# Kernel optimization log

Measured on AMD Instinct MI355X. Metric: run time of the kernel, lower is better.

The kernel has to match this reference:

```python
import jax, jax.numpy as jnp
import numpy as np

N = 8192        # total nodes in the batch of graphs
E = 262144      # edges (avg degree 32)
F_IN = 128      # input node features
G = 64          # graphs in batch
C = 10          # classes
K1, K2, K3 = 4096, 2048, 1024  # int(0.5*N), int(0.5*K1), int(0.5*K2)


def setup_inputs() -> dict:
    key = jax.random.key(0)
    ks = jax.random.split(key, 16)
    def lin(k, i, o):
        return jax.random.normal(k, (i, o), jnp.float32) / np.float32(np.sqrt(i))
    return {
        "x": jax.random.normal(ks[0], (N, F_IN), jnp.float32),
        "edge_index": jax.random.randint(ks[1], (2, E), 0, N),
        "batch": jnp.sort(jax.random.randint(ks[2], (N,), 0, G)),
        "W1": lin(ks[3], F_IN, 32), "b1": jnp.zeros((32,), jnp.float32),
        "W2": lin(ks[4], 32, 64),   "b2": jnp.zeros((64,), jnp.float32),
        "W3": lin(ks[5], 64, 128),  "b3": jnp.zeros((128,), jnp.float32),
        "W4": lin(ks[6], 128, 256), "b4": jnp.zeros((256,), jnp.float32),
        "W5": lin(ks[7], 384, 128), "b5": jnp.zeros((128,), jnp.float32),
        "W6": lin(ks[8], 192, 64),  "b6": jnp.zeros((64,), jnp.float32),
        "W7": lin(ks[9], 96, 32),   "b7": jnp.zeros((32,), jnp.float32),
        "p1": jax.random.normal(ks[10], (32,), jnp.float32),
        "p2": jax.random.normal(ks[11], (64,), jnp.float32),
        "p3": jax.random.normal(ks[12], (128,), jnp.float32),
        "Wl1": lin(ks[13], 64, 64),
        "Wc": lin(ks[14], 64, C), "bc": jnp.zeros((C,), jnp.float32),
    }


def _gcn(A, x, W, b):
    # PyG GCNConv (improved=False): out = D^-1/2 (A+I) D^-1/2 propagated src->dst.
    n = A.shape[0]
    Ah = A + jnp.eye(n, dtype=A.dtype)
    deg = Ah.sum(axis=0)                                  # degree at targets (cols)
    dinv = jnp.where(deg > 0, deg ** -0.5, 0.0).astype(A.dtype)
    An = dinv[:, None] * Ah * dinv[None, :]               # edge norm d[src]^-.5 * d[dst]^-.5
    return An.T @ (x @ W) + b                             # out[dst] += norm * (xW)[src]


def _gpool(A, x, p, k):
    # GPool: scores = Linear(x)/||p||, top-k select, gate by sigmoid, reindex dense adj.
    scores = (x @ p) / jnp.linalg.norm(p)                 # [n]
    vals, idx = jax.lax.top_k(scores, k)
    xp = x[idx] * jax.nn.sigmoid(vals)[:, None]
    Ap = (A[idx][:, idx] > 0).astype(x.dtype)             # dense_to_sparse rebinarizes
    return xp, Ap, idx


def reference(x, edge_index, batch, W1, b1, W2, b2, W3, b3, W4, b4, W5, b5,
              W6, b6, W7, b7, p1, p2, p3, Wl1, Wc, bc):
    elu = jax.nn.elu
    # to_dense_adj: dense N x N adjacency (duplicate edges accumulate)
    A = jnp.zeros((N, N), x.dtype).at[edge_index[0], edge_index[1]].add(1.0)
    x1 = elu(_gcn(A, x, W1, b1))
    x2, A2, i2 = _gpool(A, x1, p1, K1); x2 = elu(x2)
    x3 = elu(_gcn(A2, x2, W2, b2))
    x4, A4, i4 = _gpool(A2, x3, p2, K2); x4 = elu(x4)
    x5 = elu(_gcn(A4, x4, W3, b3))
    x6, A6, i6 = _gpool(A4, x5, p3, K3); x6 = elu(x6)
    x7 = elu(_gcn(A6, x6, W4, b4))
    u = jnp.zeros((K2, x7.shape[1]), x7.dtype).at[i6].set(x7)   # GUnpool
    x8 = elu(jnp.concatenate([u, x5], axis=1))
    x9 = elu(_gcn(A4, x8, W5, b5))
    u = jnp.zeros((K1, x9.shape[1]), x9.dtype).at[i4].set(x9)
    x10 = elu(jnp.concatenate([u, x3], axis=1))
    x11 = elu(_gcn(A2, x10, W6, b6))
    u = jnp.zeros((N, x11.shape[1]), x11.dtype).at[i2].set(x11)
    x12 = elu(jnp.concatenate([u, x1], axis=1))
    x13 = elu(_gcn(A, x12, W7, b7))
    gmax = jax.ops.segment_max(x13, batch, num_segments=G)      # global max pool
    gsum = jax.ops.segment_sum(x13, batch, num_segments=G)
    cnt = jax.ops.segment_sum(jnp.ones((N, 1), x13.dtype), batch, num_segments=G)
    h = elu(jnp.concatenate([gmax, gsum / cnt], axis=1))        # [G, 64]
    h = elu(h @ Wl1)
    return jax.nn.log_softmax(h @ Wc + bc, axis=-1)
```

## Files before the change

kernel.cpp:

```cpp
#include <hip/hip_runtime.h>
#include <math.h>

#define NN 8192
#define EE 262144
#define GG 64
#define CC 10
#define KK1 4096
#define KK2 2048
#define KK3 1024
#define PITCH 128

typedef unsigned long long ull;

__device__ __forceinline__ float eluf(float x) { return x > 0.f ? x : expm1f(x); }
__device__ __forceinline__ float sigf(float x) { return 1.f / (1.f + expf(-x)); }
__device__ __forceinline__ unsigned f2s(float f) {
    unsigned u = __float_as_uint(f);
    return (u & 0x80000000u) ? ~u : (u | 0x80000000u);
}

__global__ void k_init(const int* __restrict__ ei, int* __restrict__ cnt1,
                       int* __restrict__ csr1, const int* __restrict__ batch,
                       int* __restrict__ gstart, const float* __restrict__ X,
                       const float* __restrict__ W, float* __restrict__ Y) {
    __shared__ float Xs[32][33];
    __shared__ float Ws[32][36];
    int tid = threadIdx.x;
    if ((int)blockIdx.x >= 1024) {
        int txn = tid & 7, tym = tid >> 3;
        int m0 = ((int)blockIdx.x - 1024) * 32;
        float4 acc = make_float4(0.f, 0.f, 0.f, 0.f);
        for (int k0 = 0; k0 < 128; k0 += 32) {
            int r = tid >> 3, c4 = (tid & 7) << 2;
            *(float4*)&Xs[r][c4] = *(const float4*)&X[(size_t)(m0 + r) * 128 + k0 + c4];
            *(float4*)&Ws[r][c4] = *(const float4*)&W[(size_t)(k0 + r) * 32 + c4];
            __syncthreads();
#pragma unroll 8
            for (int kk = 0; kk < 32; kk++) {
                float4 wv = *(const float4*)&Ws[kk][txn * 4];
                float xv = Xs[tym][kk];
                acc.x += xv * wv.x; acc.y += xv * wv.y;
                acc.z += xv * wv.z; acc.w += xv * wv.w;
            }
            __syncthreads();
        }
        *(float4*)&Y[(size_t)(m0 + tym) * 32 + txn * 4] = acc;
        return;
    }
    int e = blockIdx.x * 256 + tid;
    int s = ei[e], d = ei[EE + e];
    int pos = atomicAdd(&cnt1[d], 1);
    csr1[(d << 7) + pos] = s;
    if (e < NN) {
        int g = batch[e];
        int prev = (e == 0) ? -1 : batch[e - 1];
        for (int gg = prev + 1; gg <= g; gg++) gstart[gg] = e;
        if (e == NN - 1)
            for (int gg = g + 1; gg <= GG; gg++) gstart[gg] = NN;
    }
}

template<int KPOOL, int F, int FOUT, int L1>
__global__ void k_pool_gemm_sub(const float* __restrict__ x, const float* __restrict__ score,
                                const int* __restrict__ idx, float* __restrict__ xW,
                                const float* __restrict__ W,
                                const int* __restrict__ csrP, const int* __restrict__ roffP,
                                const int* __restrict__ degP,
                                const int* __restrict__ invmap,
                                int* __restrict__ csrO, int* __restrict__ roffO,
                                int* __restrict__ degO, float* __restrict__ dinvO) {
    constexpr int MT = KPOOL / 32, NT = FOUT / 32, NPOOL = MT * NT;
    int tid = threadIdx.x;
    if ((int)blockIdx.x < NPOOL) {
        __shared__ float Xs[32][F + 4];
        __shared__ float Ws[32][36];
        __shared__ float sfac[32];
        __shared__ int sIdx[32];
        int mt = (int)blockIdx.x % MT, nt = (int)blockIdx.x / MT;
        int m0 = mt * 32, n0 = nt * 32;
        if (tid < 32) {
            int j = idx[m0 + tid];
            sIdx[tid] = j;
            sfac[tid] = sigf(score[j]);
        }
        __syncthreads();
        for (int i4 = tid; i4 < 32 * (F / 4); i4 += 256) {
            int r = i4 / (F / 4), c = i4 % (F / 4);
            float4 v = *(const float4*)&x[(size_t)sIdx[r] * F + c * 4];
            float sf = sfac[r];
            v.x = eluf(v.x * sf); v.y = eluf(v.y * sf);
            v.z = eluf(v.z * sf); v.w = eluf(v.w * sf);
            *(float4*)&Xs[r][c * 4] = v;
        }
        __syncthreads();
        int txn = tid & 7, tym = tid >> 3;
        float4 acc = make_float4(0.f, 0.f, 0.f, 0.f);
        for (int k0 = 0; k0 < F; k0 += 32) {
            {
                int r = tid >> 3, c4 = (tid & 7) << 2;
                *(float4*)&Ws[r][c4] = *(const float4*)&W[(size_t)(k0 + r) * FOUT + n0 + c4];
            }
            __syncthreads();
#pragma unroll 8
            for (int kk = 0; kk < 32; kk++) {
                float4 wv = *(const float4*)&Ws[kk][txn * 4];
                float xv = Xs[tym][k0 + kk];
                acc.x += xv * wv.x; acc.y += xv * wv.y;
                acc.z += xv * wv.z; acc.w += xv * wv.w;
            }
            __syncthreads();
        }
        *(float4*)&xW[(size_t)(m0 + tym) * FOUT + n0 + txn * 4] = acc;
        return;
    }
    int wid = (((int)blockIdx.x - NPOOL) * 256 + tid) >> 6;
    int lane = tid & 63;
    if (wid >= KPOOL) return;
    int j = idx[wid];
    int cnt = 0;
    if (L1) {
        int j0 = j << 7;
        int len = degP[j];
        int e0 = (lane < len) ? csrP[j0 + lane] : -1;
        int e1 = (64 + lane < len) ? csrP[j0 + 64 + lane] : -1;
        bool dup0 = false, dup1 = false;
        for (int q = 0; q < len - 1; q++) {
            int vq = (q < 64) ? __shfl(e0, q, 64) : __shfl(e1, q - 64, 64);
            if (lane > q && e0 == vq) dup0 = true;
            if (64 + lane > q && e1 == vq) dup1 = true;
        }
        {
            bool sel = (lane < len) && !dup0;
            int val = 0;
            if (sel) { int v = invmap[e0]; if (v > 0) val = v - 1; else sel = false; }
            ull m = __ballot(sel);
            if (sel) { int off = __popcll(m & ((1ull << lane) - 1ull)); csrO[j0 + cnt + off] = val; }
            cnt += __popcll(m);
        }
        {
            bool sel = (64 + lane < len) && !dup1;
            int val = 0;
            if (sel) { int v = invmap[e1]; if (v > 0) val = v - 1; else sel = false; }
            ull m = __ballot(sel);
            if (sel) { int off = __popcll(m & ((1ull << lane) - 1ull)); csrO[j0 + cnt + off] = val; }
            cnt += __popcll(m);
        }
        if (lane == 0) {
            roffO[wid] = j0;
            degO[wid] = cnt;
            dinvO[wid] = 1.f / sqrtf((float)(cnt + 1));
        }
    } else {
        int j0 = roffP[j];
        int len = degP[j];
        for (int base = 0; base < len; base += 64) {
            bool sel = false;
            int val = 0;
            if (base + lane < len) {
                int e = csrP[j0 + base + lane];
                int v = invmap[e];
                if (v > 0) { sel = true; val = v - 1; }
            }
            ull m = __ballot(sel);
            if (sel) { int off = __popcll(m & ((1ull << lane) - 1ull)); csrO[j0 + cnt + off] = val; }
            cnt += __popcll(m);
        }
        if (lane == 0) {
            roffO[wid] = j0;
            degO[wid] = cnt;
            dinvO[wid] = 1.f / sqrtf((float)(cnt + 1));
        }
    }
}

__global__ void k_gemm_up(const float* __restrict__ xl, const int* __restrict__ inv,
                          const float* __restrict__ xr, int Fl, int Fr,
                          const float* __restrict__ W, float* __restrict__ Y,
                          int M, int K, int F) {
    __shared__ float Xs[32][33];
    __shared__ float Ws[32][36];
    __shared__ int sIdx[32];
    int tid = threadIdx.x;
    int txn = tid & 7, tym = tid >> 3;
    int m0 = blockIdx.x * 32, n0 = blockIdx.y * 32;
    if (tid < 32) sIdx[tid] = inv[m0 + tid];
    float4 acc = make_float4(0.f, 0.f, 0.f, 0.f);
    __syncthreads();
    for (int k0 = 0; k0 < K; k0 += 32) {
        {
            int r = tid >> 3, c4 = (tid & 7) << 2;
            int kk = k0 + c4;
            float4 v;
            if (kk < Fl) {
                int rr = sIdx[r];
                v = (rr > 0) ? *(const float4*)&xl[(size_t)(rr - 1) * Fl + kk]
                             : make_float4(0.f, 0.f, 0.f, 0.f);
            } else {
                v = *(const float4*)&xr[(size_t)(m0 + r) * Fr + (kk - Fl)];
            }
            v.x = eluf(v.x); v.y = eluf(v.y); v.z = eluf(v.z); v.w = eluf(v.w);
            *(float4*)&Xs[r][c4] = v;
            *(float4*)&Ws[r][c4] = *(const float4*)&W[(size_t)(k0 + r) * F + n0 + c4];
        }
        __syncthreads();
#pragma unroll 8
        for (int kk = 0; kk < 32; kk++) {
            float4 wv = *(const float4*)&Ws[kk][txn * 4];
            float xv = Xs[tym][kk];
            acc.x += xv * wv.x; acc.y += xv * wv.y;
            acc.z += xv * wv.z; acc.w += xv * wv.w;
        }
        __syncthreads();
    }
    *(float4*)&Y[(size_t)(m0 + tym) * F + n0 + txn * 4] = acc;
}

template<int LOGF, int SCORE, int L1, int LS>
__global__ void k_prop(const int* __restrict__ csr, const int* __restrict__ roff,
                       const int* __restrict__ deg, const float* __restrict__ dinv,
                       const float* __restrict__ xW, const float* __restrict__ b,
                       float* __restrict__ xout, const float* __restrict__ p,
                       float* __restrict__ score) {
    constexpr int FQ = 1 << (LOGF - 2);
    constexpr int S = 1 << LS;
    constexpr int RL = FQ * S;
    const float4* xW4 = (const float4*)xW;
    int t = blockIdx.x * 256 + threadIdx.x;
    int d = t >> (LOGF - 2 + LS);
    int rem = t & (RL - 1);
    int q = rem >> LS, h = rem & (S - 1);
    int j0 = L1 ? (d << 7) : roff[d];
    int dg = deg[d];
    int j1 = j0 + dg;
    float dd = L1 ? (1.f / sqrtf((float)(dg + 1))) : dinv[d];
    int idx = (d << (LOGF - 2)) + q;
    float4 sum;
    if (h == 0) {
        float4 v0 = xW4[idx];
        sum = make_float4(dd * v0.x, dd * v0.y, dd * v0.z, dd * v0.w);
    } else {
        sum = make_float4(0.f, 0.f, 0.f, 0.f);
    }
    for (int j = j0 + h; j < j1; j += S) {
        int s = csr[j];
        float ds = L1 ? (1.f / sqrtf((float)(deg[s] + 1))) : dinv[s];
        float4 xv = xW4[(s << (LOGF - 2)) + q];
        sum.x += ds * xv.x; sum.y += ds * xv.y;
        sum.z += ds * xv.z; sum.w += ds * xv.w;
    }
#pragma unroll
    for (int m = 1; m < S; m <<= 1) {
        sum.x += __shfl_xor(sum.x, m, 64);
        sum.y += __shfl_xor(sum.y, m, 64);
        sum.z += __shfl_xor(sum.z, m, 64);
        sum.w += __shfl_xor(sum.w, m, 64);
    }
    float4 bv = *(const float4*)&b[q << 2];
    float4 o;
    o.x = eluf(dd * sum.x + bv.x);
    o.y = eluf(dd * sum.y + bv.y);
    o.z = eluf(dd * sum.z + bv.z);
    o.w = eluf(dd * sum.w + bv.w);
    if (h == 0) ((float4*)xout)[idx] = o;
    if (SCORE) {
        float4 pv = *(const float4*)&p[q << 2];
        float sc = 0.f, nr = 0.f;
        if (h == 0) {
            sc = o.x * pv.x + o.y * pv.y + o.z * pv.z + o.w * pv.w;
            nr = pv.x * pv.x + pv.y * pv.y + pv.z * pv.z + pv.w * pv.w;
        }
#pragma unroll
        for (int m = RL >> 1; m >= 1; m >>= 1) {
            sc += __shfl_xor(sc, m, 64);
            nr += __shfl_xor(nr, m, 64);
        }
        if (rem == 0) score[d] = sc / sqrtf(nr);
    }
}

__device__ __forceinline__ ull cex_shfl(ull v, int st, bool takeMax) {
    ull pv = __shfl_xor(v, st, 64);
    return takeMax ? (v > pv ? v : pv) : (v < pv ? v : pv);
}
__device__ __forceinline__ void cexr(ull& a, ull& b, bool desc) {
    if (desc ? (a < b) : (a > b)) { ull x = a; a = b; b = x; }
}

__global__ void k_topk_f(const float* __restrict__ score, ull* __restrict__ keys,
                         int N, int k, int* __restrict__ out_idx,
                         int* __restrict__ invmap, int* __restrict__ ctr) {
    __shared__ ull sk[4096];
    int tid = threadIdx.x;
    int bid = blockIdx.x;
    int nb = N >> 11;
    {
        int base = bid << 11;
        int giA = base + tid, giB = giA + 1024;
        ull a = ((ull)f2s(score[giA]) << 32) | (unsigned)(~giA);
        ull b = ((ull)f2s(score[giB]) << 32) | (unsigned)(~giB);
        for (int sz = 2; sz <= 2048; sz <<= 1) {
            int st = sz >> 1;
            if (st >= 64) {
                sk[tid] = a; sk[tid + 1024] = b;
                __syncthreads();
                for (; st >= 64; st >>= 1) {
                    int i = ((tid & ~(st - 1)) << 1) | (tid & (st - 1));
                    int j = i | st;
                    ull u = sk[i], v = sk[j];
                    bool desc = (((base + i) & sz) == 0);
                    if (desc ? (u < v) : (u > v)) { sk[i] = v; sk[j] = u; }
                    __syncthreads();
                }
                a = sk[tid]; b = sk[tid + 1024];
            }
            for (; st >= 1; st >>= 1) {
                bool low = (tid & st) == 0;
                a = cex_shfl(a, st, ((giA & sz) == 0) == low);
                b = cex_shfl(b, st, ((giB & sz) == 0) == low);
            }
        }
        if (nb == 1) {
            if (giA < k) { int j = (int)(~(unsigned)(a & 0xFFFFFFFFu)); out_idx[giA] = j; invmap[j] = giA + 1; }
            if (giB < k) { int j = (int)(~(unsigned)(b & 0xFFFFFFFFu)); out_idx[giB] = j; invmap[j] = giB + 1; }
            return;
        }
        keys[giA] = a; keys[giB] = b;
    }
    __syncthreads();
    if (tid == 0) { __threadfence(); atomicAdd(ctr, 1); }

    if (N == 4096) {
        if (bid != 0) return;
        if (tid == 0) { while (atomicAdd(ctr, 0) < 2) ; __threadfence(); }
        __syncthreads();
        ull a0 = keys[tid],        a1 = keys[tid + 1024];
        ull a2 = keys[tid + 2048], a3 = keys[tid + 3072];
        cexr(a0, a2, true); cexr(a1, a3, true);
        sk[tid] = a0; sk[tid + 1024] = a1;
        __syncthreads();
        for (int st = 1024; st >= 64; st >>= 1) {
            int i = ((tid & ~(st - 1)) << 1) | (tid & (st - 1));
            int j = i | st;
            ull u = sk[i], v = sk[j];
            if (u < v) { sk[i] = v; sk[j] = u; }
            __syncthreads();
        }
        a0 = sk[tid]; a1 = sk[tid + 1024];
        for (int st = 32; st >= 1; st >>= 1) {
            bool low = (tid & st) == 0;
            a0 = cex_shfl(a0, st, low);
            a1 = cex_shfl(a1, st, low);
        }
        int p, j;
        p = tid;        j = (int)(~(unsigned)(a0 & 0xFFFFFFFFu)); out_idx[p] = j; invmap[j] = p + 1;
        p = tid + 1024; j = (int)(~(unsigned)(a1 & 0xFFFFFFFFu)); out_idx[p] = j; invmap[j] = p + 1;
        return;
    }

    if (bid >= 2) return;
    if (tid == 0) { while (atomicAdd(ctr, 0) < 4) ; __threadfence(); }
    __syncthreads();
    {
        int base = bid << 12;
        bool desc = ((base & 4096) == 0);
        ull k0 = keys[base + tid], k1 = keys[base + tid + 1024];
        ull k2 = keys[base + tid + 2048], k3 = keys[base + tid + 3072];
        cexr(k0, k2, desc); cexr(k1, k3, desc);
        sk[tid] = k0; sk[tid + 1024] = k1; sk[tid + 2048] = k2; sk[tid + 3072] = k3;
        __syncthreads();
        for (int st = 1024; st >= 64; st >>= 1) {
            for (int pp = tid; pp < 2048; pp += 1024) {
                int i = ((pp & ~(st - 1)) << 1) | (pp & (st - 1));
                int j = i | st;
                ull u = sk[i], v = sk[j];
                if (desc ? (u < v) : (u > v)) { sk[i] = v; sk[j] = u; }
            }
            __syncthreads();
        }
        k0 = sk[tid]; k1 = sk[tid + 1024]; k2 = sk[tid + 2048]; k3 = sk[tid + 3072];
        for (int st = 32; st >= 1; st >>= 1) {
            bool low = (tid & st) == 0;
            k0 = cex_shfl(k0, st, desc == low);
            k1 = cex_shfl(k1, st, desc == low);
            k2 = cex_shfl(k2, st, desc == low);
            k3 = cex_shfl(k3, st, desc == low);
        }
        keys[base + tid] = k0; keys[base + tid + 1024] = k1;
        keys[base + tid + 2048] = k2; keys[base + tid + 3072] = k3;
    }
    __syncthreads();
    if (tid == 0) { __threadfence(); atomicAdd(ctr, 1); }
    if (bid != 0) return;
    if (tid == 0) { while (atomicAdd(ctr, 0) < 6) ; __threadfence(); }
    __syncthreads();
    {
        ull a0 = keys[tid],        a1 = keys[tid + 1024];
        ull a2 = keys[tid + 2048], a3 = keys[tid + 3072];
        ull b0 = keys[tid + 4096], b1 = keys[tid + 5120];
        ull b2 = keys[tid + 6144], b3 = keys[tid + 7168];
        cexr(a0, b0, true); cexr(a1, b1, true);
        cexr(a2, b2, true); cexr(a3, b3, true);
        cexr(a0, a2, true); cexr(a1, a3, true);
        sk[tid] = a0; sk[tid + 1024] = a1; sk[tid + 2048] = a2; sk[tid + 3072] = a3;
        __syncthreads();
        for (int st = 1024; st >= 64; st >>= 1) {
            for (int pp = tid; pp < 2048; pp += 1024) {
                int i = ((pp & ~(st - 1)) << 1) | (pp & (st - 1));
                int j = i | st;
                ull u = sk[i], v = sk[j];
                if (u < v) { sk[i] = v; sk[j] = u; }
            }
            __syncthreads();
        }
        a0 = sk[tid]; a1 = sk[tid + 1024]; a2 = sk[tid + 2048]; a3 = sk[tid + 3072];
        for (int st = 32; st >= 1; st >>= 1) {
            bool low = (tid & st) == 0;
            a0 = cex_shfl(a0, st, low);
            a1 = cex_shfl(a1, st, low);
            a2 = cex_shfl(a2, st, low);
            a3 = cex_shfl(a3, st, low);
        }
        int p, j;
        p = tid;        j = (int)(~(unsigned)(a0 & 0xFFFFFFFFu)); out_idx[p] = j; invmap[j] = p + 1;
        p = tid + 1024; j = (int)(~(unsigned)(a1 & 0xFFFFFFFFu)); out_idx[p] = j; invmap[j] = p + 1;
        p = tid + 2048; j = (int)(~(unsigned)(a2 & 0xFFFFFFFFu)); out_idx[p] = j; invmap[j] = p + 1;
        p = tid + 3072; j = (int)(~(unsigned)(a3 & 0xFFFFFFFFu)); out_idx[p] = j; invmap[j] = p + 1;
    }
}

__global__ void k_finale(const float* __restrict__ x13, const int* __restrict__ gstart,
                         const float* __restrict__ Wl1, const float* __restrict__ Wc,
                         const float* __restrict__ bc, float* __restrict__ out) {
    __shared__ float sm[8][32], ss[8][32];
    __shared__ float h0[64], h1[64], lg[CC];
    int g = blockIdx.x;
    int j0 = gstart[g], j1 = gstart[g + 1];
    int t = threadIdx.x;
    int f = t & 31, r = t >> 5;
    float m = -INFINITY, s = 0.f;
    for (int j = j0 + r; j < j1; j += 8) {
        float v = x13[(j << 5) + f];
        m = fmaxf(m, v);
        s += v;
    }
    sm[r][f] = m; ss[r][f] = s;
    __syncthreads();
    if (t < 32) {
        float mm = sm[0][t], sss = ss[0][t];
        for (int i = 1; i < 8; i++) { mm = fmaxf(mm, sm[i][t]); sss += ss[i][t]; }
        h0[t] = eluf(mm);
        h0[32 + t] = eluf(sss / (float)(j1 - j0));
    }
    __syncthreads();
    if (t < 64) {
        float sum = 0.f;
        for (int kk = 0; kk < 64; kk++) sum += h0[kk] * Wl1[kk * 64 + t];
        h1[t] = eluf(sum);
    }
    __syncthreads();
    if (t < CC) {
        float sum = bc[t];
        for (int kk = 0; kk < 64; kk++) sum += h1[kk] * Wc[kk * CC + t];
        lg[t] = sum;
    }
    __syncthreads();
    if (t == 0) {
        float mm = -1e30f;
        for (int c = 0; c < CC; c++) mm = fmaxf(mm, lg[c]);
        float se = 0.f;
        for (int c = 0; c < CC; c++) se += expf(lg[c] - mm);
        float lse = mm + logf(se);
        for (int c = 0; c < CC; c++) out[g * CC + c] = lg[c] - lse;
    }
}

extern "C" void kernel_launch(void* const* d_in, const int* in_sizes, int n_in,
                              void* d_out, int out_size, void* d_ws, size_t ws_size,
                              hipStream_t stream) {
    const float* x = (const float*)d_in[0];
    const int* ei = (const int*)d_in[1];
    const int* batch = (const int*)d_in[2];
    const float* W1 = (const float*)d_in[3];  const float* b1 = (const float*)d_in[4];
    const float* W2 = (const float*)d_in[5];  const float* b2 = (const float*)d_in[6];
    const float* W3 = (const float*)d_in[7];  const float* b3 = (const float*)d_in[8];
    const float* W4 = (const float*)d_in[9];  const float* b4 = (const float*)d_in[10];
    const float* W5 = (const float*)d_in[11]; const float* b5 = (const float*)d_in[12];
    const float* W6 = (const float*)d_in[13]; const float* b6 = (const float*)d_in[14];
    const float* W7 = (const float*)d_in[15]; const float* b7 = (const float*)d_in[16];
    const float* p1 = (const float*)d_in[17];
    const float* p2 = (const float*)d_in[18];
    const float* p3 = (const float*)d_in[19];
    const float* Wl1 = (const float*)d_in[20];
    const float* Wc = (const float*)d_in[21];
    const float* bc = (const float*)d_in[22];
    float* out = (float*)d_out;
    (void)in_sizes; (void)n_in; (void)out_size; (void)ws_size;

    char* w = (char*)d_ws;
    size_t off = 0;
    auto alloc = [&](size_t bytes) -> char* {
        char* p = w + off;
        off = (off + bytes + 255) & ~(size_t)255;
        return p;
    };

    size_t zero_begin = off;
    int* cnt1 = (int*)alloc(NN * 4);
    int* pos2 = (int*)alloc(NN * 4);
    int* inv4 = (int*)alloc(KK1 * 4);
    int* inv6 = (int*)alloc(KK2 * 4);
    int* tkctr = (int*)alloc(2 * 4);
    size_t zero_len = off - zero_begin;

    float* dinv2 = (float*)alloc(KK1 * 4);
    float* dinv3 = (float*)alloc(KK2 * 4);
    float* dinv4 = (float*)alloc(KK3 * 4);
    int* roff2 = (int*)alloc(KK1 * 4); int* deg2 = (int*)alloc(KK1 * 4);
    int* roff3 = (int*)alloc(KK2 * 4); int* deg3 = (int*)alloc(KK2 * 4);
    int* roff4 = (int*)alloc(KK3 * 4); int* deg4 = (int*)alloc(KK3 * 4);
    int* csr1 = (int*)alloc((size_t)NN * PITCH * 4);
    int* csr2 = (int*)alloc((size_t)NN * PITCH * 4);
    int* csr3 = (int*)alloc((size_t)NN * PITCH * 4);
    int* csr4 = (int*)alloc((size_t)NN * PITCH * 4);
    float* xW = (float*)alloc((size_t)262144 * 4);
    float* x1 = (float*)alloc((size_t)NN * 32 * 4);
    float* x3 = (float*)alloc((size_t)KK1 * 64 * 4);
    float* x5 = (float*)alloc((size_t)KK2 * 128 * 4);
    float* x7 = (float*)alloc((size_t)KK3 * 256 * 4);
    float* x9 = (float*)alloc((size_t)KK2 * 128 * 4);
    float* x11 = (float*)alloc((size_t)KK1 * 64 * 4);
    float* x13 = (float*)alloc((size_t)NN * 32 * 4);
    float* score1 = (float*)alloc(NN * 4);
    float* score2 = (float*)alloc(KK1 * 4);
    float* score3 = (float*)alloc(KK2 * 4);
    int* i2 = (int*)alloc(KK1 * 4);
    int* i4 = (int*)alloc(KK2 * 4);
    int* i6 = (int*)alloc(KK3 * 4);
    ull* keys = (ull*)alloc((size_t)NN * 8);
    int* gstart = (int*)alloc((GG + 1) * 4);

    hipMemsetAsync(w + zero_begin, 0, zero_len, stream);

    const int B = 256;
    k_init<<<1280, B, 0, stream>>>(ei, cnt1, csr1, batch, gstart, x, W1, xW);

    k_prop<5, 1, 1, 3><<<2048, B, 0, stream>>>(csr1, nullptr, cnt1, nullptr, xW, b1,
                                               x1, p1, score1);

    k_topk_f<<<4, 1024, 0, stream>>>(score1, keys, NN, KK1, i2, pos2, tkctr);
    k_pool_gemm_sub<KK1, 32, 64, 1><<<256 + KK1 / 4, B, 0, stream>>>(
        x1, score1, i2, xW, W2, csr1, nullptr, cnt1, pos2, csr2, roff2, deg2, dinv2);

    k_prop<6, 1, 0, 2><<<1024, B, 0, stream>>>(csr2, roff2, deg2, dinv2, xW, b2,
                                               x3, p2, score2);

    k_topk_f<<<2, 1024, 0, stream>>>(score2, keys, KK1, KK2, i4, inv4, tkctr + 1);
    k_pool_gemm_sub<KK2, 64, 128, 0><<<256 + KK2 / 4, B, 0, stream>>>(
        x3, score2, i4, xW, W3, csr2, roff2, deg2, inv4, csr3, roff3, deg3, dinv3);

    k_prop<7, 1, 0, 1><<<512, B, 0, stream>>>(csr3, roff3, deg3, dinv3, xW, b3,
                                              x5, p3, score3);

    k_topk_f<<<1, 1024, 0, stream>>>(score3, keys, KK2, KK3, i6, inv6, nullptr);
    k_pool_gemm_sub<KK3, 128, 256, 0><<<256 + KK3 / 4, B, 0, stream>>>(
        x5, score3, i6, xW, W4, csr3, roff3, deg3, inv6, csr4, roff4, deg4, dinv4);

    k_prop<8, 0, 0, 1><<<512, B, 0, stream>>>(csr4, roff4, deg4, dinv4, xW, b4,
                                              x7, nullptr, nullptr);

    k_gemm_up<<<dim3(KK2 / 32, 4), B, 0, stream>>>(x7, inv6, x5, 256, 128,
                                                   W5, xW, KK2, 384, 128);
    k_prop<7, 0, 0, 2><<<1024, B, 0, stream>>>(csr3, roff3, deg3, dinv3, xW, b5,
                                               x9, nullptr, nullptr);

    k_gemm_up<<<dim3(KK1 / 32, 2), B, 0, stream>>>(x9, inv4, x3, 128, 64,
                                                   W6, xW, KK1, 192, 64);
    k_prop<6, 0, 0, 2><<<1024, B, 0, stream>>>(csr2, roff2, deg2, dinv2, xW, b6,
                                               x11, nullptr, nullptr);

    k_gemm_up<<<dim3(NN / 32, 1), B, 0, stream>>>(x11, pos2, x1, 64, 32,
                                                  W7, xW, NN, 96, 32);
    k_prop<5, 0, 1, 3><<<2048, B, 0, stream>>>(csr1, nullptr, cnt1, nullptr, xW, b7,
                                               x13, nullptr, nullptr);

    k_finale<<<GG, B, 0, stream>>>(x13, gstart, Wl1, Wc, bc, out);
}
```

Before: 310.3 us.

## Fuse final GCN propagation with per-graph pooling and classifier head

Result: slower. 366.3 us (+18.0%).

```diff
diff --git a/kernel.cpp b/kernel.cpp
--- a/kernel.cpp
+++ b/kernel.cpp
@@ -275,6 +275,119 @@
             nr += __shfl_xor(nr, m, 64);
         }
         if (rem == 0) score[d] = sc / sqrtf(nr);
+    }
+}
+
+__global__ void k_prop7(const int* __restrict__ csr, const int* __restrict__ deg,
+                        const float* __restrict__ xW, const float* __restrict__ b,
+                        float* __restrict__ x13, const int* __restrict__ batch,
+                        const int* __restrict__ gstart, int* __restrict__ garr,
+                        const float* __restrict__ Wl1, const float* __restrict__ Wc,
+                        const float* __restrict__ bc, float* __restrict__ out) {
+    const float4* xW4 = (const float4*)xW;
+    int tid = threadIdx.x;
+    int t = blockIdx.x * 256 + tid;
+    int d = t >> 6;
+    int rem = t & 63;
+    int q = rem >> 3, h = rem & 7;
+    int j0 = d << 7;
+    int dg = deg[d];
+    int j1 = j0 + dg;
+    float dd = 1.f / sqrtf((float)(dg + 1));
+    int idx = (d << 3) + q;
+    float4 sum;
+    if (h == 0) {
+        float4 v0 = xW4[idx];
+        sum = make_float4(dd * v0.x, dd * v0.y, dd * v0.z, dd * v0.w);
+    } else {
+        sum = make_float4(0.f, 0.f, 0.f, 0.f);
+    }
+    for (int j = j0 + h; j < j1; j += 8) {
+        int s = csr[j];
+        float ds = 1.f / sqrtf((float)(deg[s] + 1));
+        float4 xv = xW4[(s << 3) + q];
+        sum.x += ds * xv.x; sum.y += ds * xv.y;
+        sum.z += ds * xv.z; sum.w += ds * xv.w;
+    }
+#pragma unroll
+    for (int m = 1; m < 8; m <<= 1) {
+        sum.x += __shfl_xor(sum.x, m, 64);
+        sum.y += __shfl_xor(sum.y, m, 64);
+        sum.z += __shfl_xor(sum.z, m, 64);
+        sum.w += __shfl_xor(sum.w, m, 64);
+    }
+    float4 bv = *(const float4*)&b[q << 2];
+    float4 o;
+    o.x = eluf(dd * sum.x + bv.x);
+    o.y = eluf(dd * sum.y + bv.y);
+    o.z = eluf(dd * sum.z + bv.z);
+    o.w = eluf(dd * sum.w + bv.w);
+    if (h == 0) ((float4*)x13)[idx] = o;
+
+    __shared__ int doneG[4];
+    __shared__ int nDone;
+    __shared__ float sm[8][32], ss[8][32];
+    __shared__ float h0s[64], h1s[64], lgs[CC];
+    if (tid == 0) nDone = 0;
+    __syncthreads();
+    if (tid == 0) {
+        __threadfence();
+        int r0 = blockIdx.x << 2;
+        int g0 = batch[r0], g1 = batch[r0 + 3];
+        int nd = 0;
+        for (int g = g0; g <= g1; g++) {
+            int lo = gstart[g] > r0 ? gstart[g] : r0;
+            int hi = gstart[g + 1] < r0 + 4 ? gstart[g + 1] : r0 + 4;
+            int c = hi - lo;
+            int tot = gstart[g + 1] - gstart[g];
+            if (c > 0 && atomicAdd(&garr[g], c) + c == tot) {
+                __threadfence();
+                doneG[nd++] = g;
+            }
+        }
+        nDone = nd;
+    }
+    __syncthreads();
+    for (int ii = 0; ii < nDone; ii++) {
+        int g = doneG[ii];
+        int j0g = gstart[g], j1g = gstart[g + 1];
+        int f = tid & 31, r = tid >> 5;
+        float m = -INFINITY, s = 0.f;
+        for (int j = j0g + r; j < j1g; j += 8) {
+            float v = x13[(j << 5) + f];
+            m = fmaxf(m, v);
+            s += v;
+        }
+        sm[r][f] = m; ss[r][f] = s;
+        __syncthreads();
+        if (tid < 32) {
+            float mm = sm[0][tid], sss = ss[0][tid];
+            for (int i = 1; i < 8; i++) { mm = fmaxf(mm, sm[i][tid]); sss += ss[i][tid]; }
+            h0s[tid] = eluf(mm);
+            h0s[32 + tid] = eluf(sss / (float)(j1g - j0g));
+        }
+        __syncthreads();
+        if (tid < 64) {
+            float sumv = 0.f;
+            for (int kk = 0; kk < 64; kk++) sumv += h0s[kk] * Wl1[kk * 64 + tid];
+            h1s[tid] = eluf(sumv);
+        }
+        __syncthreads();
+        if (tid < CC) {
+            float sumv = bc[tid];
+            for (int kk = 0; kk < 64; kk++) sumv += h1s[kk] * Wc[kk * CC + tid];
+            lgs[tid] = sumv;
+        }
+        __syncthreads();
+        if (tid == 0) {
+            float mm = -1e30f;
+            for (int c = 0; c < CC; c++) mm = fmaxf(mm, lgs[c]);
+            float se = 0.f;
+            for (int c = 0; c < CC; c++) se += expf(lgs[c] - mm);
+            float lse = mm + logf(se);
+            for (int c = 0; c < CC; c++) out[g * CC + c] = lgs[c] - lse;
+        }
+        __syncthreads();
     }
 }
 
@@ -428,52 +541,6 @@
     }
 }
 
-__global__ void k_finale(const float* __restrict__ x13, const int* __restrict__ gstart,
-                         const float* __restrict__ Wl1, const float* __restrict__ Wc,
-                         const float* __restrict__ bc, float* __restrict__ out) {
-    __shared__ float sm[8][32], ss[8][32];
-    __shared__ float h0[64], h1[64], lg[CC];
-    int g = blockIdx.x;
-    int j0 = gstart[g], j1 = gstart[g + 1];
-    int t = threadIdx.x;
-    int f = t & 31, r = t >> 5;
-    float m = -INFINITY, s = 0.f;
-    for (int j = j0 + r; j < j1; j += 8) {
-        float v = x13[(j << 5) + f];
-        m = fmaxf(m, v);
-        s += v;
-    }
-    sm[r][f] = m; ss[r][f] = s;
-    __syncthreads();
-    if (t < 32) {
-        float mm = sm[0][t], sss = ss[0][t];
-        for (int i = 1; i < 8; i++) { mm = fmaxf(mm, sm[i][t]); sss += ss[i][t]; }
-        h0[t] = eluf(mm);
-        h0[32 + t] = eluf(sss / (float)(j1 - j0));
-    }
-    __syncthreads();
-    if (t < 64) {
-        float sum = 0.f;
-        for (int kk = 0; kk < 64; kk++) sum += h0[kk] * Wl1[kk * 64 + t];
-        h1[t] = eluf(sum);
-    }
-    __syncthreads();
-    if (t < CC) {
-        float sum = bc[t];
-        for (int kk = 0; kk < 64; kk++) sum += h1[kk] * Wc[kk * CC + t];
-        lg[t] = sum;
-    }
-    __syncthreads();
-    if (t == 0) {
-        float mm = -1e30f;
-        for (int c = 0; c < CC; c++) mm = fmaxf(mm, lg[c]);
-        float se = 0.f;
-        for (int c = 0; c < CC; c++) se += expf(lg[c] - mm);
-        float lse = mm + logf(se);
-        for (int c = 0; c < CC; c++) out[g * CC + c] = lg[c] - lse;
-    }
-}
-
 extern "C" void kernel_launch(void* const* d_in, const int* in_sizes, int n_in,
                               void* d_out, int out_size, void* d_ws, size_t ws_size,
                               hipStream_t stream) {
@@ -510,6 +577,7 @@
     int* inv4 = (int*)alloc(KK1 * 4);
     int* inv6 = (int*)alloc(KK2 * 4);
     int* tkctr = (int*)alloc(2 * 4);
+    int* garr = (int*)alloc(GG * 4);
     size_t zero_len = off - zero_begin;
 
     float* dinv2 = (float*)alloc(KK1 * 4);
@@ -580,8 +648,6 @@
 
     k_gemm_up<<<dim3(NN / 32, 1), B, 0, stream>>>(x11, pos2, x1, 64, 32,
                                                   W7, xW, NN, 96, 32);
-    k_prop<5, 0, 1, 3><<<2048, B, 0, stream>>>(csr1, nullptr, cnt1, nullptr, xW, b7,
-                                               x13, nullptr, nullptr);
-
-    k_finale<<<GG, B, 0, stream>>>(x13, gstart, Wl1, Wc, bc, out);
-}
+    k_prop7<<<2048, B, 0, stream>>>(csr1, cnt1, xW, b7, x13, batch, gstart, garr,
+                                    Wl1, Wc, bc, out);
+}
```
